# Kernel tuning notes

Measured on AMD Instinct MI355X. Metric: run time of the kernel, lower is better.

The kernel has to match this reference:

```python
import jax, jax.numpy as jnp
import numpy as np

NF4 = jnp.array([-1.0, -0.6961928009986877, -0.5250730514526367, -0.39491748809814453,
                 -0.28444138169288635, -0.18477343022823334, -0.09105003625154495, 0.0,
                 0.07958029955625534, 0.16093020141124725, 0.24611230194568634,
                 0.33791524171829224, 0.44070982933044434, 0.5626170039176941,
                 0.7229568362236023, 1.0], dtype=jnp.float32)
BLOCK_SIZE = 64
SCALING = 32.0 / 16.0  # alpha / rank


def setup_inputs() -> dict:
    key = jax.random.key(0)
    k = jax.random.split(key, 6)
    B, S, IN, OUT, R = 4, 128, 4096, 11008, 16
    n_blocks = (OUT * IN) // BLOCK_SIZE  # 704512, exact (no padding needed)
    return {
        "x": jax.random.normal(k[0], (B, S, IN), jnp.float32),
        "weight_indices": jax.random.randint(k[1], (OUT, IN), 0, 16, dtype=jnp.int32),
        "weight_scales": jax.random.uniform(k[2], (n_blocks,), jnp.float32),
        "lora_A": jax.random.normal(k[3], (IN, R), jnp.float32),
        "lora_B": jax.random.normal(k[4], (R, OUT), jnp.float32),
        "bias": jax.random.normal(k[5], (OUT,), jnp.float32),
    }


def dequantize_nf4(indices, scales, shape):
    # LUT gather then blockwise absmax scale
    w = NF4[indices.reshape(-1)]                    # [out*in]
    w = w.reshape(-1, BLOCK_SIZE) * scales[:, None]  # [n_blocks, block]
    return w.reshape(shape)                          # [out, in]


def reference(x, weight_indices, weight_scales, lora_A, lora_B, bias):
    W = dequantize_nf4(weight_indices, weight_scales, weight_indices.shape)  # [out, in]
    base = jnp.einsum("bsi,oi->bso", x, W) + bias                            # F.linear
    lora = (x @ lora_A) @ lora_B                                             # low-rank path (dropout p=0 -> identity)
    return base + lora * SCALING
```

## Files before the change

kernel.cpp:

```cpp
#include <hip/hip_runtime.h>
#include <stdint.h>

typedef __bf16 bf16x8 __attribute__((ext_vector_type(8)));
typedef float f32x4 __attribute__((ext_vector_type(4)));
typedef unsigned short ushort_t;

#define N_OUT 11008
#define K_DIM 4096
#define M_DIM 512
#define BM 256
#define BN 64
#define BK 64
#define KHALF 2048
#define NT 32

__constant__ float c_nf4[16] = {
    -1.0f, -0.6961928009986877f, -0.5250730514526367f, -0.39491748809814453f,
    -0.28444138169288635f, -0.18477343022823334f, -0.09105003625154495f, 0.0f,
    0.07958029955625534f, 0.16093020141124725f, 0.24611230194568634f,
    0.33791524171829224f, 0.44070982933044434f, 0.5626170039176941f,
    0.7229568362236023f, 1.0f};

__device__ __forceinline__ uint32_t pkbf(float lo, float hi) {
  uint32_t ul = __builtin_bit_cast(uint32_t, lo);
  uint32_t uh = __builtin_bit_cast(uint32_t, hi);
  return ((ul + 0x8000u) >> 16) | ((uh + 0x8000u) & 0xffff0000u);
}

__device__ __forceinline__ void async16(const void* g, void* l) {
  __builtin_amdgcn_global_load_lds(
      (const __attribute__((address_space(1))) void*)g,
      (__attribute__((address_space(3))) void*)l, 16, 0, 0);
}

__device__ __forceinline__ bf16x8 ldfrag(const ushort_t* p) {
  uint4 r = *reinterpret_cast<const uint4*>(p);
  return __builtin_bit_cast(bf16x8, r);
}

__device__ __forceinline__ uint32_t dq2(int a, int b, float s, const float2* lut) {
  float2 l = lut[a | (b << 4)];
  return pkbf(l.x * s, l.y * s);
}

__global__ void k_prep(const float* __restrict__ x, const float* __restrict__ lA,
                       const float* __restrict__ lB, const float* __restrict__ bias,
                       ushort_t* __restrict__ xbf, ushort_t* __restrict__ xap,
                       ushort_t* __restrict__ btp, float* __restrict__ out) {
  const int b = blockIdx.x, t = threadIdx.x;
  if (b < 1024) {
    int oc = b * 256 + t;
    int m = oc >> 9;
    int cr = oc & 511;
    int win = cr >> 3, cp = cr & 7;
    int c = cp ^ (m & 7);
    const float4* s4 = (const float4*)(x + (size_t)m * K_DIM + win * 64 + c * 8);
    float4 v0 = s4[0], v1 = s4[1];
    uint4 o;
    o.x = pkbf(v0.x, v0.y);
    o.y = pkbf(v0.z, v0.w);
    o.z = pkbf(v1.x, v1.y);
    o.w = pkbf(v1.z, v1.w);
    ((uint4*)xbf)[oc] = o;
  } else if (b < 1536) {
    __shared__ float red[256 * 17];
    int m = b - 1024;
    int ks = t * 16;
    alignas(16) float xs[16];
    const f32x4* xv = (const f32x4*)(x + (size_t)m * K_DIM + ks);
    ((f32x4*)xs)[0] = xv[0];
    ((f32x4*)xs)[1] = xv[1];
    ((f32x4*)xs)[2] = xv[2];
    ((f32x4*)xs)[3] = xv[3];
    f32x4 ac0 = 0.f, ac1 = 0.f, ac2 = 0.f, ac3 = 0.f;
#pragma unroll
    for (int kk = 0; kk < 16; ++kk) {
      float xk = xs[kk];
      const f32x4* l4 = (const f32x4*)(lA + (size_t)(ks + kk) * 16);
      ac0 += xk * l4[0];
      ac1 += xk * l4[1];
      ac2 += xk * l4[2];
      ac3 += xk * l4[3];
    }
#pragma unroll
    for (int r = 0; r < 4; ++r) {
      red[t * 17 + r] = ac0[r];
      red[t * 17 + 4 + r] = ac1[r];
      red[t * 17 + 8 + r] = ac2[r];
      red[t * 17 + 12 + r] = ac3[r];
    }
    __syncthreads();
#pragma unroll
    for (int s = 128; s >= 16; s >>= 1) {
      if (t < s)
        for (int r = 0; r < 16; ++r) red[t * 17 + r] += red[(t + s) * 17 + r];
      __syncthreads();
    }
    if (t < 32) {
      float v = 0.f;
      if (t < 16) {
        for (int p = 0; p < 16; ++p) v += red[p * 17 + t];
        v *= 2.0f;
      }
      uint32_t u = __builtin_bit_cast(uint32_t, v);
      xap[(size_t)m * 32 + t] = (ushort_t)((u + 0x8000u) >> 16);
    }
  } else if (b < 1579) {
    int o = (b - 1536) * 256 + t;
    uint32_t p[8];
#pragma unroll
    for (int j = 0; j < 8; ++j)
      p[j] = pkbf(lB[(size_t)(2 * j) * N_OUT + o], lB[(size_t)(2 * j + 1) * N_OUT + o]);
    uint4* dst = reinterpret_cast<uint4*>(btp + (size_t)o * 32);
    dst[0] = make_uint4(p[0], p[1], p[2], p[3]);
    dst[1] = make_uint4(p[4], p[5], p[6], p[7]);
    dst[2] = make_uint4(0u, 0u, 0u, 0u);
    dst[3] = make_uint4(0u, 0u, 0u, 0u);
  } else {
    int i = (b - 1579) * 256 + t;
    int col4 = i % 2752;
    ((float4*)out)[i] = ((const float4*)bias)[col4];
  }
}

__launch_bounds__(256, 3)
__global__ void k_main(const ushort_t* __restrict__ xbf, const int* __restrict__ wi,
                       const float* __restrict__ sc, const ushort_t* __restrict__ xap,
                       const ushort_t* __restrict__ btp, float* __restrict__ out) {
  __shared__ __align__(16) ushort_t lds_a[BM * BK];
  __shared__ __align__(16) ushort_t lds_b[2][BN * 72];
  __shared__ float2 lutp[256];

  const int t = threadIdx.x;
  const int lane = t & 63;
  const int w = t >> 6;

  const int n = blockIdx.x;
  const int wg = (n & 7) * 86 + (n >> 3);
  const int o0 = (wg >> 2) * BN;
  const int kh = (wg >> 1) & 1;
  const int m0 = (wg & 1) * BM;
  const int k0 = kh * KHALF;

  lutp[t] = make_float2(c_nf4[t & 15], c_nf4[t >> 4]);

  const int brow = t >> 2, bq = t & 3;
  const int* gb = wi + (size_t)(o0 + brow) * K_DIM + k0 + bq * 16;
  const float* gs = sc + (size_t)(o0 + brow) * 64 + kh * 32;
  ushort_t* lb = &lds_b[0][brow * 72 + bq * 16];
  const int bstride = BN * 72;

  const ushort_t* ga =
      xbf + (size_t)(m0 + w * 64 + (lane >> 3)) * K_DIM + k0 + (lane & 7) * 8;
  ushort_t* la_dst = lds_a + w * 4096 + lane * 8;

  f32x4 acc[4][4];
#pragma unroll
  for (int mi = 0; mi < 4; ++mi)
#pragma unroll
    for (int ni = 0; ni < 4; ++ni) acc[mi][ni] = (f32x4){0.f, 0.f, 0.f, 0.f};

  __syncthreads();

#pragma unroll
  for (int j = 0; j < 8; ++j) async16(ga + (size_t)j * 8 * K_DIM, la_dst + j * 512);
  __builtin_amdgcn_sched_barrier(0);
  int4 bi0 = ((const int4*)gb)[0], bi1 = ((const int4*)gb)[1];
  int4 bi2 = ((const int4*)gb)[2], bi3 = ((const int4*)gb)[3];
  float s = gs[0];
  gb += BK;
  uint4 braw;

  const ushort_t* afb = lds_a + (w * 64 + (lane & 15)) * BK;
  const int q = lane >> 4;
  const ushort_t* bfb = &lds_b[0][(lane & 15) * 72 + q * 8];

#pragma unroll 1
  for (int kt = 0; kt < NT; ++kt) {
    uint4 w0, w1;
    w0.x = dq2(bi0.x, bi0.y, s, lutp);
    w0.y = dq2(bi0.z, bi0.w, s, lutp);
    w0.z = dq2(bi1.x, bi1.y, s, lutp);
    w0.w = dq2(bi1.z, bi1.w, s, lutp);
    w1.x = dq2(bi2.x, bi2.y, s, lutp);
    w1.y = dq2(bi2.z, bi2.w, s, lutp);
    w1.z = dq2(bi3.x, bi3.y, s, lutp);
    w1.w = dq2(bi3.z, bi3.w, s, lutp);
    ushort_t* lbk = lb + (kt & 1) * bstride;
    *reinterpret_cast<uint4*>(lbk) = w0;
    *reinterpret_cast<uint4*>(lbk + 8) = w1;

    __syncthreads();

    const ushort_t* bfbk = bfb + (kt & 1) * bstride;
#pragma unroll
    for (int kc = 0; kc < 2; ++kc) {
      const int cpr = ((kc * 4 + q) ^ (lane & 7)) * 8;
      bf16x8 av[4], bv[4];
#pragma unroll
      for (int mi = 0; mi < 4; ++mi) av[mi] = ldfrag(afb + mi * 16 * BK + cpr);
#pragma unroll
      for (int ni = 0; ni < 4; ++ni) bv[ni] = ldfrag(bfbk + ni * 16 * 72 + kc * 32);
      if (kc == 1) {
        asm volatile("s_waitcnt lgkmcnt(0)" ::: "memory");
        if (kt + 1 < NT) {
#pragma unroll
          for (int j = 0; j < 8; ++j)
            async16(ga + (size_t)j * 8 * K_DIM + (kt + 1) * BK, la_dst + j * 512);
          __builtin_amdgcn_sched_barrier(0);
          bi0 = ((const int4*)gb)[0];
          bi1 = ((const int4*)gb)[1];
          bi2 = ((const int4*)gb)[2];
          bi3 = ((const int4*)gb)[3];
          s = gs[kt + 1];
          gb += BK;
        } else if (kh == 1) {
          braw = *reinterpret_cast<const uint4*>(btp + (size_t)(o0 + brow) * 32 + bq * 8);
        }
      }
#pragma unroll
      for (int mi = 0; mi < 4; ++mi)
#pragma unroll
        for (int ni = 0; ni < 4; ++ni)
          acc[mi][ni] = __builtin_amdgcn_mfma_f32_16x16x32_bf16(av[mi], bv[ni],
                                                                acc[mi][ni], 0, 0, 0);
    }
  }

  if (kh == 1) {
    __syncthreads();
    *reinterpret_cast<uint4*>(&lds_b[0][brow * 72 + bq * 8]) = braw;
#pragma unroll
    for (int j = 0; j < 4; ++j)
      async16(xap + (size_t)(m0 + w * 64 + j * 16 + (lane >> 2)) * 32 + (lane & 3) * 8,
              lds_a + w * 2048 + j * 512 + lane * 8);
    __syncthreads();
    bf16x8 av[4], bv[4];
#pragma unroll
    for (int mi = 0; mi < 4; ++mi)
      av[mi] = ldfrag(lds_a + w * 2048 + (mi * 16 + (lane & 15)) * 32 + q * 8);
#pragma unroll
    for (int ni = 0; ni < 4; ++ni)
      bv[ni] = ldfrag(&lds_b[0][(ni * 16 + (lane & 15)) * 72 + q * 8]);
#pragma unroll
    for (int mi = 0; mi < 4; ++mi)
#pragma unroll
      for (int ni = 0; ni < 4; ++ni)
        acc[mi][ni] = __builtin_amdgcn_mfma_f32_16x16x32_bf16(av[mi], bv[ni],
                                                              acc[mi][ni], 0, 0, 0);
  }

  const int cl = lane & 15, rg = q * 4;
#pragma unroll
  for (int ni = 0; ni < 4; ++ni) {
    int col = o0 + ni * 16 + cl;
#pragma unroll
    for (int mi = 0; mi < 4; ++mi) {
      int row0 = m0 + w * 64 + mi * 16 + rg;
      float* op = out + (size_t)row0 * N_OUT + col;
#pragma unroll
      for (int i = 0; i < 4; ++i) atomicAdd(op + (size_t)i * N_OUT, acc[mi][ni][i]);
    }
  }
}

extern "C" void kernel_launch(void* const* d_in, const int* in_sizes, int n_in,
                              void* d_out, int out_size, void* d_ws, size_t ws_size,
                              hipStream_t stream) {
  const float* x = (const float*)d_in[0];
  const int* wi = (const int*)d_in[1];
  const float* sc = (const float*)d_in[2];
  const float* lA = (const float*)d_in[3];
  const float* lB = (const float*)d_in[4];
  const float* bias = (const float*)d_in[5];
  float* out = (float*)d_out;

  char* wsb = (char*)d_ws;
  ushort_t* xbf = (ushort_t*)wsb;
  ushort_t* xap = (ushort_t*)(wsb + (4u << 20));
  ushort_t* btp = (ushort_t*)(wsb + (4u << 20) + (32u << 10));

  k_prep<<<7083, 256, 0, stream>>>(x, lA, lB, bias, xbf, xap, btp, out);
  k_main<<<688, 256, 0, stream>>>(xbf, wi, sc, xap, btp, out);
}
```

Before: 363.4 us.

## Deepen weight-index prefetch to two tiles with split vmcnt waits

Unrolls the K loop by two and keeps two register sets of NF4 index and scale data, so index loads are issued two tiles ahead. The full __syncthreads is replaced by an LDS wait, a raw s_barrier and vmcnt(5), so the in-flight index loads for the next-next tile no longer block the barrier. The goal is to hide global load latency of the int32 weight stream behind MFMA work. In exchange it uses more registers, which may affect occupancy at 3 waves per SIMD. The last iteration also issues an A prefetch one tile past the K half, which reads memory the kernel does not need.

```diff
diff --git a/kernel.cpp b/kernel.cpp
--- a/kernel.cpp
+++ b/kernel.cpp
@@ -13,6 +13,7 @@
 #define BK 64
 #define KHALF 2048
 #define NT 32
+#define BSTRIDE (BN * 72)
 
 __constant__ float c_nf4[16] = {
     -1.0f, -0.6961928009986877f, -0.5250730514526367f, -0.39491748809814453f,
@@ -123,12 +124,77 @@
   }
 }
 
+__device__ __forceinline__ void tile_step(
+    int kt, int pb, int4 (&bi)[4], float& s, const float2* lutp, ushort_t* lb,
+    const ushort_t* bfb, const ushort_t* afb, const ushort_t* ga,
+    ushort_t* la_dst, const int* gb0, const float* gs, int lane, int q,
+    f32x4 (&acc)[4][4]) {
+  uint4 w0, w1;
+  w0.x = dq2(bi[0].x, bi[0].y, s, lutp);
+  w0.y = dq2(bi[0].z, bi[0].w, s, lutp);
+  w0.z = dq2(bi[1].x, bi[1].y, s, lutp);
+  w0.w = dq2(bi[1].z, bi[1].w, s, lutp);
+  w1.x = dq2(bi[2].x, bi[2].y, s, lutp);
+  w1.y = dq2(bi[2].z, bi[2].w, s, lutp);
+  w1.z = dq2(bi[3].x, bi[3].y, s, lutp);
+  w1.w = dq2(bi[3].z, bi[3].w, s, lutp);
+  *reinterpret_cast<uint4*>(lb + pb * BSTRIDE) = w0;
+  *reinterpret_cast<uint4*>(lb + pb * BSTRIDE + 8) = w1;
+  asm volatile("s_waitcnt lgkmcnt(0)" ::: "memory");
+  __builtin_amdgcn_s_barrier();
+  asm volatile("s_waitcnt vmcnt(5)" ::: "memory");
+
+  const ushort_t* bfbk = bfb + pb * BSTRIDE;
+  {
+    const int cpr = (q ^ (lane & 7)) * 8;
+    bf16x8 av[4], bv[4];
+#pragma unroll
+    for (int mi = 0; mi < 4; ++mi) av[mi] = ldfrag(afb + mi * 16 * BK + cpr);
+#pragma unroll
+    for (int ni = 0; ni < 4; ++ni) bv[ni] = ldfrag(bfbk + ni * 16 * 72);
+#pragma unroll
+    for (int mi = 0; mi < 4; ++mi)
+#pragma unroll
+      for (int ni = 0; ni < 4; ++ni)
+        acc[mi][ni] = __builtin_amdgcn_mfma_f32_16x16x32_bf16(av[mi], bv[ni],
+                                                              acc[mi][ni], 0, 0, 0);
+  }
+  {
+    const int cpr = ((4 + q) ^ (lane & 7)) * 8;
+    bf16x8 av[4], bv[4];
+#pragma unroll
+    for (int mi = 0; mi < 4; ++mi) av[mi] = ldfrag(afb + mi * 16 * BK + cpr);
+#pragma unroll
+    for (int ni = 0; ni < 4; ++ni) bv[ni] = ldfrag(bfbk + ni * 16 * 72 + 32);
+    asm volatile("s_waitcnt lgkmcnt(0)" ::: "memory");
+    __builtin_amdgcn_sched_barrier(0);
+#pragma unroll
+    for (int j = 0; j < 8; ++j)
+      async16(ga + (size_t)j * 8 * K_DIM + (size_t)(kt + 1) * BK, la_dst + j * 512);
+    __builtin_amdgcn_sched_barrier(0);
+    const int ksc = (kt + 2 < NT) ? kt + 2 : NT - 1;
+    const int4* gbk = (const int4*)(gb0 + (size_t)ksc * BK);
+    bi[0] = gbk[0];
+    bi[1] = gbk[1];
+    bi[2] = gbk[2];
+    bi[3] = gbk[3];
+    s = gs[ksc];
+    __builtin_amdgcn_sched_barrier(0);
+#pragma unroll
+    for (int mi = 0; mi < 4; ++mi)
+#pragma unroll
+      for (int ni = 0; ni < 4; ++ni)
+        acc[mi][ni] = __builtin_amdgcn_mfma_f32_16x16x32_bf16(av[mi], bv[ni],
+                                                              acc[mi][ni], 0, 0, 0);
+  }
+}
+
 __launch_bounds__(256, 3)
 __global__ void k_main(const ushort_t* __restrict__ xbf, const int* __restrict__ wi,
                        const float* __restrict__ sc, const ushort_t* __restrict__ xap,
                        const ushort_t* __restrict__ btp, float* __restrict__ out) {
   __shared__ __align__(16) ushort_t lds_a[BM * BK];
-  __shared__ __align__(16) ushort_t lds_b[2][BN * 72];
+  __shared__ __align__(16) ushort_t lds_b[2][BSTRIDE];
   __shared__ float2 lutp[256];
 
   const int t = threadIdx.x;
@@ -145,10 +211,9 @@
   lutp[t] = make_float2(c_nf4[t & 15], c_nf4[t >> 4]);
 
   const int brow = t >> 2, bq = t & 3;
-  const int* gb = wi + (size_t)(o0 + brow) * K_DIM + k0 + bq * 16;
+  const int* gb0 = wi + (size_t)(o0 + brow) * K_DIM + k0 + bq * 16;
   const float* gs = sc + (size_t)(o0 + brow) * 64 + kh * 32;
   ushort_t* lb = &lds_b[0][brow * 72 + bq * 16];
-  const int bstride = BN * 72;
 
   const ushort_t* ga =
       xbf + (size_t)(m0 + w * 64 + (lane >> 3)) * K_DIM + k0 + (lane & 7) * 8;
@@ -160,74 +225,46 @@
 #pragma unroll
     for (int ni = 0; ni < 4; ++ni) acc[mi][ni] = (f32x4){0.f, 0.f, 0.f, 0.f};
 
-  __syncthreads();
-
+  int4 biA[4], biB[4];
+  float sA, sB;
+  {
+    const int4* g0 = (const int4*)gb0;
+    biA[0] = g0[0];
+    biA[1] = g0[1];
+    biA[2] = g0[2];
+    biA[3] = g0[3];
+    sA = gs[0];
+  }
+  __builtin_amdgcn_sched_barrier(0);
 #pragma unroll
   for (int j = 0; j < 8; ++j) async16(ga + (size_t)j * 8 * K_DIM, la_dst + j * 512);
   __builtin_amdgcn_sched_barrier(0);
-  int4 bi0 = ((const int4*)gb)[0], bi1 = ((const int4*)gb)[1];
-  int4 bi2 = ((const int4*)gb)[2], bi3 = ((const int4*)gb)[3];
-  float s = gs[0];
-  gb += BK;
-  uint4 braw;
+  {
+    const int4* g1 = (const int4*)(gb0 + BK);
+    biB[0] = g1[0];
+    biB[1] = g1[1];
+    biB[2] = g1[2];
+    biB[3] = g1[3];
+    sB = gs[1];
+  }
+  __builtin_amdgcn_sched_barrier(0);
+  asm volatile("s_waitcnt lgkmcnt(0)" ::: "memory");
+  __builtin_amdgcn_s_barrier();
 
   const ushort_t* afb = lds_a + (w * 64 + (lane & 15)) * BK;
   const int q = lane >> 4;
   const ushort_t* bfb = &lds_b[0][(lane & 15) * 72 + q * 8];
 
 #pragma unroll 1
-  for (int kt = 0; kt < NT; ++kt) {
-    uint4 w0, w1;
-    w0.x = dq2(bi0.x, bi0.y, s, lutp);
-    w0.y = dq2(bi0.z, bi0.w, s, lutp);
-    w0.z = dq2(bi1.x, bi1.y, s, lutp);
-    w0.w = dq2(bi1.z, bi1.w, s, lutp);
-    w1.x = dq2(bi2.x, bi2.y, s, lutp);
-    w1.y = dq2(bi2.z, bi2.w, s, lutp);
-    w1.z = dq2(bi3.x, bi3.y, s, lutp);
-    w1.w = dq2(bi3.z, bi3.w, s, lutp);
-    ushort_t* lbk = lb + (kt & 1) * bstride;
-    *reinterpret_cast<uint4*>(lbk) = w0;
-    *reinterpret_cast<uint4*>(lbk + 8) = w1;
-
-    __syncthreads();
-
-    const ushort_t* bfbk = bfb + (kt & 1) * bstride;
-#pragma unroll
-    for (int kc = 0; kc < 2; ++kc) {
-      const int cpr = ((kc * 4 + q) ^ (lane & 7)) * 8;
-      bf16x8 av[4], bv[4];
-#pragma unroll
-      for (int mi = 0; mi < 4; ++mi) av[mi] = ldfrag(afb + mi * 16 * BK + cpr);
-#pragma unroll
-      for (int ni = 0; ni < 4; ++ni) bv[ni] = ldfrag(bfbk + ni * 16 * 72 + kc * 32);
-      if (kc == 1) {
-        asm volatile("s_waitcnt lgkmcnt(0)" ::: "memory");
-        if (kt + 1 < NT) {
-#pragma unroll
-          for (int j = 0; j < 8; ++j)
-            async16(ga + (size_t)j * 8 * K_DIM + (kt + 1) * BK, la_dst + j * 512);
-          __builtin_amdgcn_sched_barrier(0);
-          bi0 = ((const int4*)gb)[0];
-          bi1 = ((const int4*)gb)[1];
-          bi2 = ((const int4*)gb)[2];
-          bi3 = ((const int4*)gb)[3];
-          s = gs[kt + 1];
-          gb += BK;
-        } else if (kh == 1) {
-          braw = *reinterpret_cast<const uint4*>(btp + (size_t)(o0 + brow) * 32 + bq * 8);
-        }
-      }
-#pragma unroll
-      for (int mi = 0; mi < 4; ++mi)
-#pragma unroll
-        for (int ni = 0; ni < 4; ++ni)
-          acc[mi][ni] = __builtin_amdgcn_mfma_f32_16x16x32_bf16(av[mi], bv[ni],
-                                                                acc[mi][ni], 0, 0, 0);
-    }
-  }
+  for (int kt2 = 0; kt2 < NT / 2; ++kt2) {
+    tile_step(2 * kt2, 0, biA, sA, lutp, lb, bfb, afb, ga, la_dst, gb0, gs, lane, q, acc);
+    tile_step(2 * kt2 + 1, 1, biB, sB, lutp, lb, bfb, afb, ga, la_dst, gb0, gs, lane, q, acc);
+  }
+
+  asm volatile("s_waitcnt vmcnt(0)" ::: "memory");
 
   if (kh == 1) {
+    uint4 braw = *reinterpret_cast<const uint4*>(btp + (size_t)(o0 + brow) * 32 + bq * 8);
     __syncthreads();
     *reinterpret_cast<uint4*>(&lds_b[0][brow * 72 + bq * 8]) = braw;
 #pragma unroll
@@ -250,7 +287,7 @@
                                                               acc[mi][ni], 0, 0, 0);
   }
 
-  const int cl = lane & 15, rg = q * 4;
+  const int cl = lane & 15, rg = (lane >> 4) * 4;
 #pragma unroll
   for (int ni = 0; ni < 4; ++ni) {
     int col = o0 + ni * 16 + cl;
```

Result: no change. 369.2 us (+1.6%).
